# Performance work log

Measured on AMD Instinct MI355X. Metric: run time of the kernel, lower is better.

Reference implementation:

```python
import jax, jax.numpy as jnp
import numpy as np

WINDOW = 16  # hardcoded in module __init__

B, S, E, H = 2, 2048, 1024, 16
HD = E // H


def setup_inputs() -> dict:
    key = jax.random.key(0)
    k1, k2, k3, k4, k5, k6 = jax.random.split(key, 6)
    input_embeddings = jax.random.normal(k1, (B, S, E), dtype=jnp.float32)
    token_ids = jax.random.randint(k2, (B, S), 0, 32000, dtype=jnp.int64)
    # nn.MultiheadAttention parameters: packed in_proj (3E, E) + bias, out_proj (E, E) + bias
    in_proj_weight = jax.random.normal(k3, (3 * E, E), dtype=jnp.float32) * 0.02
    in_proj_bias = jax.random.normal(k4, (3 * E,), dtype=jnp.float32) * 0.02
    out_proj_weight = jax.random.normal(k5, (E, E), dtype=jnp.float32) * 0.02
    out_proj_bias = jax.random.normal(k6, (E,), dtype=jnp.float32) * 0.02
    return {
        "input_embeddings": input_embeddings,
        "token_ids": token_ids,
        "in_proj_weight": in_proj_weight,
        "in_proj_bias": in_proj_bias,
        "out_proj_weight": out_proj_weight,
        "out_proj_bias": out_proj_bias,
    }


def _blocked_mask(seq_len: int) -> jnp.ndarray:
    # Module sets mask[i, j] = True for j in [i - WINDOW, i] (17 positions).
    # PyTorch bool attn_mask: True = NOT allowed to attend.
    i = jnp.arange(seq_len)[:, None]
    j = jnp.arange(seq_len)[None, :]
    return (j <= i) & (j >= i - WINDOW)  # [S, S] bool, True = masked out


def reference(input_embeddings, token_ids, in_proj_weight, in_proj_bias,
              out_proj_weight, out_proj_bias):
    x = input_embeddings  # [B, S, E]
    b, s, e = x.shape
    # Packed QKV projection (torch Linear: y = x W^T + b)
    qkv = jnp.einsum('bse,fe->bsf', x, in_proj_weight) + in_proj_bias  # [B, S, 3E]
    q, k, v = jnp.split(qkv, 3, axis=-1)
    # Split heads: [B, H, S, HD]
    q = q.reshape(b, s, H, HD).transpose(0, 2, 1, 3)
    k = k.reshape(b, s, H, HD).transpose(0, 2, 1, 3)
    v = v.reshape(b, s, H, HD).transpose(0, 2, 1, 3)
    scale = 1.0 / jnp.sqrt(jnp.asarray(HD, dtype=x.dtype))
    scores = jnp.einsum('bhqd,bhkd->bhqk', q * scale, k)  # [B, H, S, S]
    blocked = _blocked_mask(s)  # True = masked
    scores = jnp.where(blocked[None, None, :, :], -jnp.inf, scores)
    attn = jax.nn.softmax(scores, axis=-1)
    ctx = jnp.einsum('bhqk,bhkd->bhqd', attn, v)  # [B, H, S, HD]
    ctx = ctx.transpose(0, 2, 1, 3).reshape(b, s, e)
    out = jnp.einsum('bse,fe->bsf', ctx, out_proj_weight) + out_proj_bias
    return out
```

## Files before the change

### kernel.cpp

```cpp
#include <hip/hip_runtime.h>

typedef __attribute__((ext_vector_type(8))) __bf16 bf16x8;
typedef __attribute__((ext_vector_type(4))) float f32x4;
typedef __attribute__((ext_vector_type(16))) float f32x16;
typedef unsigned short u16;
typedef unsigned int u32;

#define MFMA16(a, b, c) __builtin_amdgcn_mfma_f32_16x16x32_bf16((a), (b), (c), 0, 0, 0)
#define MFMA32(a, b, c) __builtin_amdgcn_mfma_f32_32x32x16_bf16((a), (b), (c), 0, 0, 0)

__device__ __forceinline__ u16 f2bf(float f) {
  return (u16)((__float_as_uint(f) + 0x8000u) >> 16);
}

#define BDIM 2
#define SDIM 2048
#define EDIM 1024
#define HDIM 16
#define HD 64
#define MDIM (BDIM * SDIM)

#define SC_C1 0.1803368801111355f

typedef __attribute__((address_space(3))) void lds_void;
typedef __attribute__((address_space(1))) void g_void;

__device__ __forceinline__ void async_lds16(const void* g, void* lds_byte) {
  __builtin_amdgcn_global_load_lds((const g_void*)g, (lds_void*)lds_byte, 16, 0, 0);
}

__global__ __launch_bounds__(256) void cvt3_kernel(
    const float* __restrict__ s0, u16* __restrict__ d0, int n0,
    const float* __restrict__ s1, u16* __restrict__ d1, int n1,
    const float* __restrict__ s2, u16* __restrict__ d2, int n2) {
  int i = (blockIdx.x * 256 + threadIdx.x) * 8;
  const float* s;
  u16* d;
  if (i < n0) {
    s = s0 + i; d = d0 + i;
  } else if (i < n0 + n1) {
    s = s1 + (i - n0); d = d1 + (i - n0);
  } else if (i < n0 + n1 + n2) {
    s = s2 + (i - n0 - n1); d = d2 + (i - n0 - n1);
  } else {
    return;
  }
  float4 f0 = *(const float4*)(s);
  float4 f1 = *(const float4*)(s + 4);
  union { uint4 u; u16 h[8]; } o;
  o.h[0] = f2bf(f0.x); o.h[1] = f2bf(f0.y); o.h[2] = f2bf(f0.z); o.h[3] = f2bf(f0.w);
  o.h[4] = f2bf(f1.x); o.h[5] = f2bf(f1.y); o.h[6] = f2bf(f1.z); o.h[7] = f2bf(f1.w);
  *(uint4*)(d) = o.u;
}

__global__ __launch_bounds__(256) void gemm_qkv_kernel(
    const u16* __restrict__ X, const u16* __restrict__ W,
    const float* __restrict__ bias, u16* __restrict__ qb,
    u16* __restrict__ kb, u16* __restrict__ vtb) {
  __shared__ __align__(16) u16 As[128 * 64];
  __shared__ __align__(16) u16 Bs[128 * 64];
  const int m0 = blockIdx.x * 128, n0 = blockIdx.y * 128;
  const bool isV = (n0 >= 2 * EDIM);
  const int t = threadIdx.x;
  const int l = t & 63;
  const int quad = l >> 4, col = l & 15;
  const int wid = t >> 6;
  const int mh = wid & 1, nh = wid >> 1;
  const int wofs = (t & 192) << 4;
  f32x4 acc[4][4] = {};
  const u16* Ab = X + (size_t)m0 * EDIM;
  const u16* Bb = W + (size_t)n0 * EDIM;
  char* AsB = (char*)As;
  char* BsB = (char*)Bs;

  for (int k0 = 0; k0 < EDIM; k0 += 64) {
    __syncthreads();
#pragma unroll
    for (int p = 0; p < 4; p++) {
      int idx = p * 256 + t;
      int row = idx >> 3;
      int gch = (idx & 7) ^ (row & 7);
      async_lds16(Ab + (size_t)row * EDIM + k0 + gch * 8, AsB + p * 4096 + wofs);
      async_lds16(Bb + (size_t)row * EDIM + k0 + gch * 8, BsB + p * 4096 + wofs);
    }
    __syncthreads();
#pragma unroll
    for (int kk = 0; kk < 2; kk++) {
      bf16x8 af[4], bfr[4];
#pragma unroll
      for (int i = 0; i < 4; i++) {
        int ra = 64 * mh + 16 * i + col;
        af[i] = *(const bf16x8*)&As[ra * 64 + (((kk * 4 + quad) ^ (ra & 7)) * 8)];
        int rb = 64 * nh + 16 * i + col;
        bfr[i] = *(const bf16x8*)&Bs[rb * 64 + (((kk * 4 + quad) ^ (rb & 7)) * 8)];
      }
      if (isV) {
#pragma unroll
        for (int i = 0; i < 4; i++)
#pragma unroll
          for (int j = 0; j < 4; j++)
            acc[i][j] = MFMA16(bfr[i], af[j], acc[i][j]);
      } else {
#pragma unroll
        for (int i = 0; i < 4; i++)
#pragma unroll
          for (int j = 0; j < 4; j++)
            acc[i][j] = MFMA16(af[i], bfr[j], acc[i][j]);
      }
    }
  }

  if (isV) {
#pragma unroll
    for (int i = 0; i < 4; i++)
#pragma unroll
      for (int j = 0; j < 4; j++)
#pragma unroll
        for (int r = 0; r < 4; r++) {
          int n = n0 + 64 * nh + 16 * i + quad * 4 + r;
          int m = m0 + 64 * mh + 16 * j + col;
          float val = acc[i][j][r] + bias[n];
          int e = n & 1023;
          int hh = e >> 6, d = e & 63;
          int bb = m >> 11, s = m & 2047;
          vtb[(((size_t)(bb * HDIM + hh)) * HD + d) * SDIM + s] = f2bf(val);
        }
  } else {
    const float qscale = (n0 < EDIM) ? SC_C1 : 1.0f;
#pragma unroll
    for (int i = 0; i < 4; i++)
#pragma unroll
      for (int j = 0; j < 4; j++)
#pragma unroll
        for (int r = 0; r < 4; r++) {
          int m = m0 + 64 * mh + 16 * i + quad * 4 + r;
          int n = n0 + 64 * nh + 16 * j + col;
          float val = (acc[i][j][r] + bias[n]) * qscale;
          int which = n >> 10, e = n & 1023;
          int hh = e >> 6, d = e & 63;
          int bb = m >> 11, s = m & 2047;
          u16* dst = (which == 0) ? qb : kb;
          dst[(((size_t)(bb * HDIM + hh)) * SDIM + s) * HD + d] = f2bf(val);
        }
  }
}

__global__ __launch_bounds__(256) void attn_kernel(
    const u16* __restrict__ qg, const u16* __restrict__ kg,
    const u16* __restrict__ vtg, u16* __restrict__ ctx) {
  __shared__ __align__(16) u16 KB[2][64 * 64];
  __shared__ __align__(16) u16 VB[3][64 * 64];

  const int bh = blockIdx.x;
  const int q0 = blockIdx.y * 128;
  const int t = threadIdx.x;
  const int wid = t >> 6, l = t & 63;
  const int col = l & 31, half = l >> 5;
  const size_t base = (size_t)bh * SDIM * HD;

  const int qw0 = q0 + 32 * wid;
  const int qi = qw0 + col;

  bf16x8 bq[4];
  {
    const u16* qp = qg + base + (size_t)qi * HD + half * 8;
#pragma unroll
    for (int f = 0; f < 4; f++) bq[f] = *(const bf16x8*)(qp + f * 16);
  }
  asm volatile("" : "+v"(bq[0]), "+v"(bq[1]), "+v"(bq[2]), "+v"(bq[3]));

  const int srow = t >> 3;
  const int g = (t & 7) ^ (srow & 7);
  const u16* kptr = kg + base + (size_t)srow * HD + g * 8;
  const u16* vptr = vtg + base + (size_t)srow * SDIM + g * 8;
  const int wofs = (t & 192) << 4;

  auto stageK = [&](int kt, int buf) {
    char* d = (char*)KB[buf] + wofs;
    async_lds16(kptr + (size_t)(kt * 64) * HD, d);
    async_lds16(kptr + (size_t)(kt * 64 + 32) * HD, d + 4096);
  };
  auto stageV = [&](int kt, int buf) {
    char* d = (char*)VB[buf] + wofs;
    async_lds16(vptr + kt * 64, d);
    async_lds16(vptr + (size_t)32 * SDIM + kt * 64, d + 4096);
  };

  auto qkt = [&](const u16* Kt, f32x16 (&sco)[2]) {
#pragma unroll
    for (int s = 0; s < 2; s++)
#pragma unroll
      for (int f = 0; f < 4; f++) {
        int kr = 32 * s + col;
        int phys = (2 * f + half) ^ (kr & 7);
        bf16x8 kf = *(const bf16x8*)&Kt[kr * 64 + phys * 8];
        sco[s] = MFMA32(kf, bq[f], sco[s]);
      }
  };

  float ps0 = 0.f, ps1 = 0.f, ps2 = 0.f, ps3 = 0.f;
  f32x16 oacc[2] = {};

  auto smax = [&](int kt, f32x16 (&cur)[2], bool band, u32 (&w)[2][8]) {
#pragma unroll
    for (int s = 0; s < 2; s++) {
      float p[16];
#pragma unroll
      for (int r = 0; r < 16; r++) {
        float v = cur[s][r];
        if (band) {
          int j = kt * 64 + 32 * s + (r & 3) + 8 * (r >> 2) + 4 * half;
          if (j <= qi && j + 16 >= qi) v = -1.0e30f;
        }
        p[r] = __builtin_exp2f(v);
      }
#pragma unroll
      for (int r = 0; r < 16; r++) {
        if ((r & 3) == 0) ps0 += p[r];
        else if ((r & 3) == 1) ps1 += p[r];
        else if ((r & 3) == 2) ps2 += p[r];
        else ps3 += p[r];
      }
#pragma unroll
      for (int j = 0; j < 8; j++) {
        u32 wv;
        asm("v_cvt_pk_bf16_f32 %0, %1, %2" : "=v"(wv) : "v"(p[2 * j]), "v"(p[2 * j + 1]));
        w[s][j] = wv;
      }
    }
  };

  auto pv = [&](const u16* Vt, u32 (&w)[2][8]) {
#pragma unroll
    for (int s = 0; s < 2; s++)
#pragma unroll
      for (int b2 = 0; b2 < 2; b2++) {
        u32 x0 = w[s][4 * b2 + 0], x1 = w[s][4 * b2 + 1];
        u32 y0 = w[s][4 * b2 + 2], y1 = w[s][4 * b2 + 3];
        asm("v_permlane32_swap_b32 %0, %1" : "+v"(x0), "+v"(y0));
        asm("v_permlane32_swap_b32 %0, %1" : "+v"(x1), "+v"(y1));
        uint4 pw;
        pw.x = x0; pw.y = x1; pw.z = y0; pw.w = y1;
        bf16x8 pa = __builtin_bit_cast(bf16x8, pw);
        int ks = 2 * s + b2;
#pragma unroll
        for (int dt = 0; dt < 2; dt++) {
          int vr = 32 * dt + col;
          int phys = (2 * ks + half) ^ (vr & 7);
          bf16x8 vf = *(const bf16x8*)&Vt[vr * 64 + phys * 8];
          oacc[dt] = MFMA32(vf, pa, oacc[dt]);
        }
      }
  };

  const int NT = SDIM / 64;

  auto body = [&](int kt, f32x16 (&cur)[2], f32x16 (&nxt)[2]) {
    __syncthreads();
    if (kt + 1 < NT) {
      nxt[0] = (f32x16){};
      nxt[1] = (f32x16){};
      qkt(KB[(kt + 1) & 1], nxt);
    }
    if (kt + 2 < NT) {
      stageK(kt + 2, kt & 1);
      stageV(kt + 2, (unsigned)(kt + 2) % 3u);
    }
    u32 w[2][8];
    bool band = (kt * 64 <= qw0 + 31) && (kt * 64 + 63 >= qw0 - 16);
    smax(kt, cur, band, w);
    pv(VB[(unsigned)kt % 3u], w);
  };

  f32x16 scA[2] = {}, scB[2] = {};
  stageK(0, 0);
  stageV(0, 0);
  __syncthreads();
  qkt(KB[0], scA);
  stageK(1, 1);
  stageV(1, 1);

#pragma unroll 1
  for (int kt = 0; kt < NT; kt += 2) {
    body(kt, scA, scB);
    body(kt + 1, scB, scA);
  }

  float psum = (ps0 + ps1) + (ps2 + ps3);
  psum += __shfl_xor(psum, 32, 64);
  float linv = 1.0f / psum;

  const int b = bh >> 4, h = bh & 15;
  u16* cbase = ctx + ((size_t)(b * SDIM + qi)) * EDIM + h * HD;
#pragma unroll
  for (int dt = 0; dt < 2; dt++)
#pragma unroll
    for (int a = 0; a < 4; a++) {
      float v0 = oacc[dt][4 * a + 0] * linv, v1 = oacc[dt][4 * a + 1] * linv;
      float v2 = oacc[dt][4 * a + 2] * linv, v3 = oacc[dt][4 * a + 3] * linv;
      u32 w0, w1;
      asm("v_cvt_pk_bf16_f32 %0, %1, %2" : "=v"(w0) : "v"(v0), "v"(v1));
      asm("v_cvt_pk_bf16_f32 %0, %1, %2" : "=v"(w1) : "v"(v2), "v"(v3));
      uint2 st;
      st.x = w0; st.y = w1;
      *(uint2*)(cbase + 32 * dt + 8 * a + 4 * half) = st;
    }
}

__global__ __launch_bounds__(256) void gemm_out_kernel(
    const u16* __restrict__ A, const u16* __restrict__ W,
    const float* __restrict__ bias, float* __restrict__ out) {
  __shared__ __align__(16) u16 As[128 * 64];
  __shared__ __align__(16) u16 Bs[128 * 64];
  const int m0 = blockIdx.x * 128, n0 = blockIdx.y * 128;
  const int t = threadIdx.x;
  const int l = t & 63;
  const int quad = l >> 4, col = l & 15;
  const int wid = t >> 6;
  const int mh = wid & 1, nh = wid >> 1;
  const int wofs = (t & 192) << 4;
  f32x4 acc[4][4] = {};
  const u16* Ab = A + (size_t)m0 * EDIM;
  const u16* Bb = W + (size_t)n0 * EDIM;
  char* AsB = (char*)As;
  char* BsB = (char*)Bs;

  for (int k0 = 0; k0 < EDIM; k0 += 64) {
    __syncthreads();
#pragma unroll
    for (int p = 0; p < 4; p++) {
      int idx = p * 256 + t;
      int row = idx >> 3;
      int gch = (idx & 7) ^ (row & 7);
      async_lds16(Ab + (size_t)row * EDIM + k0 + gch * 8, AsB + p * 4096 + wofs);
      async_lds16(Bb + (size_t)row * EDIM + k0 + gch * 8, BsB + p * 4096 + wofs);
    }
    __syncthreads();
#pragma unroll
    for (int kk = 0; kk < 2; kk++) {
      bf16x8 af[4], bfr[4];
#pragma unroll
      for (int i = 0; i < 4; i++) {
        int ra = 64 * mh + 16 * i + col;
        af[i] = *(const bf16x8*)&As[ra * 64 + (((kk * 4 + quad) ^ (ra & 7)) * 8)];
        int rb = 64 * nh + 16 * i + col;
        bfr[i] = *(const bf16x8*)&Bs[rb * 64 + (((kk * 4 + quad) ^ (rb & 7)) * 8)];
      }
#pragma unroll
      for (int i = 0; i < 4; i++)
#pragma unroll
        for (int j = 0; j < 4; j++)
          acc[i][j] = MFMA16(af[i], bfr[j], acc[i][j]);
    }
  }

#pragma unroll
  for (int i = 0; i < 4; i++)
#pragma unroll
    for (int j = 0; j < 4; j++)
#pragma unroll
      for (int r = 0; r < 4; r++) {
        int m = m0 + 64 * mh + 16 * i + quad * 4 + r;
        int n = n0 + 64 * nh + 16 * j + col;
        out[(size_t)m * EDIM + n] = acc[i][j][r] + bias[n];
      }
}

extern "C" void kernel_launch(void* const* d_in, const int* in_sizes, int n_in,
                              void* d_out, int out_size, void* d_ws,
                              size_t ws_size, hipStream_t stream) {
  const float* x = (const float*)d_in[0];
  const float* in_w = (const float*)d_in[2];
  const float* in_b = (const float*)d_in[3];
  const float* out_w = (const float*)d_in[4];
  const float* out_b = (const float*)d_in[5];
  float* out = (float*)d_out;

  char* ws = (char*)d_ws;
  u16* Xb  = (u16*)ws;
  u16* ctx = (u16*)ws;
  u16* qb  = (u16*)(ws + (size_t)( 8 << 20));
  u16* kb  = (u16*)(ws + (size_t)(16 << 20));
  u16* vtb = (u16*)(ws + (size_t)(24 << 20));
  u16* Wib = (u16*)(ws + (size_t)(32 << 20));
  u16* Wob = (u16*)(ws + (size_t)(38 << 20));

  const int nX = MDIM * EDIM;
  const int nWi = 3 * EDIM * EDIM;
  const int nWo = EDIM * EDIM;
  cvt3_kernel<<<(nX + nWi + nWo) / 8 / 256, 256, 0, stream>>>(
      x, Xb, nX, in_w, Wib, nWi, out_w, Wob, nWo);

  gemm_qkv_kernel<<<dim3(MDIM / 128, 3 * EDIM / 128), 256, 0, stream>>>(
      Xb, Wib, in_b, qb, kb, vtb);
  attn_kernel<<<dim3(BDIM * HDIM, SDIM / 128), 256, 0, stream>>>(qb, kb, vtb, ctx);
  gemm_out_kernel<<<dim3(MDIM / 128, EDIM / 128), 256, 0, stream>>>(
      ctx, Wob, out_b, out);
}
```

Measured before the change: 219.7 us.

## Split attention key tiles across wave pairs, halving query rows per block

Each attention block now covers 64 query rows instead of 128. The four waves split into two query groups times two key halves, so each wave computes one 32-key sub-tile per step, and partial outputs and row sums are reduced through LDS at the end. This doubles the grid to raise occupancy and shortens per-wave work. Plain __syncthreads are replaced by explicit vmcnt waits and barriers, and s_setprio is added around the MFMA sections. The cost is twice as many K/V tile loads per query row plus an extra LDS reduction and barrier.

```diff
diff --git a/kernel.cpp b/kernel.cpp
--- a/kernel.cpp
+++ b/kernel.cpp
@@ -145,20 +145,22 @@
   }
 }
 
-__global__ __launch_bounds__(256) void attn_kernel(
+__global__ __launch_bounds__(256, 4) void attn_kernel(
     const u16* __restrict__ qg, const u16* __restrict__ kg,
     const u16* __restrict__ vtg, u16* __restrict__ ctx) {
   __shared__ __align__(16) u16 KB[2][64 * 64];
   __shared__ __align__(16) u16 VB[3][64 * 64];
 
   const int bh = blockIdx.x;
-  const int q0 = blockIdx.y * 128;
+  const int q0 = blockIdx.y * 64;
   const int t = threadIdx.x;
   const int wid = t >> 6, l = t & 63;
   const int col = l & 31, half = l >> 5;
+  const int wq = wid & 1;
+  const int kh = wid >> 1;
   const size_t base = (size_t)bh * SDIM * HD;
 
-  const int qw0 = q0 + 32 * wid;
+  const int qw0 = q0 + 32 * wq;
   const int qi = qw0 + col;
 
   bf16x8 bq[4];
@@ -169,116 +171,118 @@
   }
   asm volatile("" : "+v"(bq[0]), "+v"(bq[1]), "+v"(bq[2]), "+v"(bq[3]));
 
-  const int srow = t >> 3;
-  const int g = (t & 7) ^ (srow & 7);
-  const u16* kptr = kg + base + (size_t)srow * HD + g * 8;
-  const u16* vptr = vtg + base + (size_t)srow * SDIM + g * 8;
-  const int wofs = (t & 192) << 4;
+  const int sr = l >> 3;
+  const int g = (l & 7) ^ sr;
+  const u16* kpt = kg + base + (size_t)(16 * wid + sr) * HD + g * 8;
+  const u16* vpt = vtg + base + (size_t)(16 * wid + sr) * SDIM + g * 8;
 
   auto stageK = [&](int kt, int buf) {
-    char* d = (char*)KB[buf] + wofs;
-    async_lds16(kptr + (size_t)(kt * 64) * HD, d);
-    async_lds16(kptr + (size_t)(kt * 64 + 32) * HD, d + 4096);
+    char* d = (char*)KB[buf] + wid * 2048;
+    async_lds16(kpt + (size_t)(kt * 64) * HD, d);
+    async_lds16(kpt + (size_t)(kt * 64 + 8) * HD, d + 1024);
   };
   auto stageV = [&](int kt, int buf) {
-    char* d = (char*)VB[buf] + wofs;
-    async_lds16(vptr + kt * 64, d);
-    async_lds16(vptr + (size_t)32 * SDIM + kt * 64, d + 4096);
-  };
-
-  auto qkt = [&](const u16* Kt, f32x16 (&sco)[2]) {
-#pragma unroll
-    for (int s = 0; s < 2; s++)
-#pragma unroll
-      for (int f = 0; f < 4; f++) {
-        int kr = 32 * s + col;
-        int phys = (2 * f + half) ^ (kr & 7);
-        bf16x8 kf = *(const bf16x8*)&Kt[kr * 64 + phys * 8];
-        sco[s] = MFMA32(kf, bq[f], sco[s]);
-      }
+    char* d = (char*)VB[buf] + wid * 2048;
+    async_lds16(vpt + kt * 64, d);
+    async_lds16(vpt + (size_t)8 * SDIM + kt * 64, d + 1024);
+  };
+
+  auto qkt = [&](const u16* Kt, f32x16& sco) {
+    const int kr = 32 * kh + col;
+    const int r7 = kr & 7;
+#pragma unroll
+    for (int f = 0; f < 4; f++) {
+      int phys = (2 * f + half) ^ r7;
+      bf16x8 kf = *(const bf16x8*)&Kt[kr * 64 + phys * 8];
+      sco = MFMA32(kf, bq[f], sco);
+    }
   };
 
   float ps0 = 0.f, ps1 = 0.f, ps2 = 0.f, ps3 = 0.f;
   f32x16 oacc[2] = {};
 
-  auto smax = [&](int kt, f32x16 (&cur)[2], bool band, u32 (&w)[2][8]) {
-#pragma unroll
-    for (int s = 0; s < 2; s++) {
-      float p[16];
-#pragma unroll
-      for (int r = 0; r < 16; r++) {
-        float v = cur[s][r];
-        if (band) {
-          int j = kt * 64 + 32 * s + (r & 3) + 8 * (r >> 2) + 4 * half;
-          if (j <= qi && j + 16 >= qi) v = -1.0e30f;
-        }
-        p[r] = __builtin_exp2f(v);
-      }
-#pragma unroll
-      for (int r = 0; r < 16; r++) {
-        if ((r & 3) == 0) ps0 += p[r];
-        else if ((r & 3) == 1) ps1 += p[r];
-        else if ((r & 3) == 2) ps2 += p[r];
-        else ps3 += p[r];
-      }
-#pragma unroll
-      for (int j = 0; j < 8; j++) {
-        u32 wv;
-        asm("v_cvt_pk_bf16_f32 %0, %1, %2" : "=v"(wv) : "v"(p[2 * j]), "v"(p[2 * j + 1]));
-        w[s][j] = wv;
-      }
-    }
-  };
-
-  auto pv = [&](const u16* Vt, u32 (&w)[2][8]) {
-#pragma unroll
-    for (int s = 0; s < 2; s++)
-#pragma unroll
-      for (int b2 = 0; b2 < 2; b2++) {
-        u32 x0 = w[s][4 * b2 + 0], x1 = w[s][4 * b2 + 1];
-        u32 y0 = w[s][4 * b2 + 2], y1 = w[s][4 * b2 + 3];
-        asm("v_permlane32_swap_b32 %0, %1" : "+v"(x0), "+v"(y0));
-        asm("v_permlane32_swap_b32 %0, %1" : "+v"(x1), "+v"(y1));
-        uint4 pw;
-        pw.x = x0; pw.y = x1; pw.z = y0; pw.w = y1;
-        bf16x8 pa = __builtin_bit_cast(bf16x8, pw);
-        int ks = 2 * s + b2;
-#pragma unroll
-        for (int dt = 0; dt < 2; dt++) {
-          int vr = 32 * dt + col;
-          int phys = (2 * ks + half) ^ (vr & 7);
-          bf16x8 vf = *(const bf16x8*)&Vt[vr * 64 + phys * 8];
-          oacc[dt] = MFMA32(vf, pa, oacc[dt]);
-        }
-      }
+  auto smax = [&](int kt, f32x16& cur, bool band, u32 (&w)[8]) {
+    float p[16];
+#pragma unroll
+    for (int r = 0; r < 16; r++) {
+      float v = cur[r];
+      if (band) {
+        int j = kt * 64 + 32 * kh + (r & 3) + 8 * (r >> 2) + 4 * half;
+        if (j <= qi && j + 16 >= qi) v = -1.0e30f;
+      }
+      p[r] = __builtin_exp2f(v);
+    }
+#pragma unroll
+    for (int r = 0; r < 16; r += 4) {
+      ps0 += p[r]; ps1 += p[r + 1]; ps2 += p[r + 2]; ps3 += p[r + 3];
+    }
+#pragma unroll
+    for (int j = 0; j < 8; j++)
+      asm("v_cvt_pk_bf16_f32 %0, %1, %2"
+          : "=v"(w[j]) : "v"(p[2 * j]), "v"(p[2 * j + 1]));
+  };
+
+  auto pv = [&](const u16* Vt, u32 (&w)[8]) {
+#pragma unroll
+    for (int b2 = 0; b2 < 2; b2++) {
+      u32 x0 = w[4 * b2 + 0], x1 = w[4 * b2 + 1];
+      u32 y0 = w[4 * b2 + 2], y1 = w[4 * b2 + 3];
+      asm("v_permlane32_swap_b32 %0, %1" : "+v"(x0), "+v"(y0));
+      asm("v_permlane32_swap_b32 %0, %1" : "+v"(x1), "+v"(y1));
+      uint4 pw;
+      pw.x = x0; pw.y = x1; pw.z = y0; pw.w = y1;
+      bf16x8 pa = __builtin_bit_cast(bf16x8, pw);
+      int ks = 2 * kh + b2;
+#pragma unroll
+      for (int dt = 0; dt < 2; dt++) {
+        int vr = 32 * dt + col;
+        int phys = (2 * ks + half) ^ (vr & 7);
+        bf16x8 vf = *(const bf16x8*)&Vt[vr * 64 + phys * 8];
+        oacc[dt] = MFMA32(vf, pa, oacc[dt]);
+      }
+    }
   };
 
   const int NT = SDIM / 64;
-
-  auto body = [&](int kt, f32x16 (&cur)[2], f32x16 (&nxt)[2]) {
-    __syncthreads();
-    if (kt + 1 < NT) {
-      nxt[0] = (f32x16){};
-      nxt[1] = (f32x16){};
-      qkt(KB[(kt + 1) & 1], nxt);
-    }
+  int vcur = 0, vstg = 2;
+
+  auto body = [&](int kt, f32x16& cur, f32x16& nxt) {
+    if (kt < NT - 1)
+      asm volatile("s_waitcnt vmcnt(2) lgkmcnt(0)" ::: "memory");
+    else
+      asm volatile("s_waitcnt vmcnt(0) lgkmcnt(0)" ::: "memory");
+    __builtin_amdgcn_s_barrier();
+    __builtin_amdgcn_sched_barrier(0);
     if (kt + 2 < NT) {
       stageK(kt + 2, kt & 1);
-      stageV(kt + 2, (unsigned)(kt + 2) % 3u);
-    }
-    u32 w[2][8];
-    bool band = (kt * 64 <= qw0 + 31) && (kt * 64 + 63 >= qw0 - 16);
+      stageV(kt + 2, vstg);
+    }
+    if (kt + 1 < NT) {
+      nxt = (f32x16){};
+      __builtin_amdgcn_s_setprio(1);
+      qkt(KB[(kt + 1) & 1], nxt);
+      __builtin_amdgcn_s_setprio(0);
+    }
+    u32 w[8];
+    bool band = (kt * 64 + 32 * kh <= qw0 + 31) &&
+                (kt * 64 + 32 * kh + 31 >= qw0 - 16);
     smax(kt, cur, band, w);
-    pv(VB[(unsigned)kt % 3u], w);
-  };
-
-  f32x16 scA[2] = {}, scB[2] = {};
+    __builtin_amdgcn_s_setprio(1);
+    pv(VB[vcur], w);
+    __builtin_amdgcn_s_setprio(0);
+    vcur = (vcur == 2) ? 0 : vcur + 1;
+    vstg = (vstg == 2) ? 0 : vstg + 1;
+  };
+
+  f32x16 scA = {}, scB = {};
   stageK(0, 0);
   stageV(0, 0);
-  __syncthreads();
-  qkt(KB[0], scA);
   stageK(1, 1);
   stageV(1, 1);
+  asm volatile("s_waitcnt vmcnt(6)" ::: "memory");
+  __builtin_amdgcn_s_barrier();
+  __builtin_amdgcn_sched_barrier(0);
+  qkt(KB[0], scA);
 
 #pragma unroll 1
   for (int kt = 0; kt < NT; kt += 2) {
@@ -286,25 +290,47 @@
     body(kt + 1, scB, scA);
   }
 
-  float psum = (ps0 + ps1) + (ps2 + ps3);
-  psum += __shfl_xor(psum, 32, 64);
-  float linv = 1.0f / psum;
-
-  const int b = bh >> 4, h = bh & 15;
-  u16* cbase = ctx + ((size_t)(b * SDIM + qi)) * EDIM + h * HD;
-#pragma unroll
-  for (int dt = 0; dt < 2; dt++)
-#pragma unroll
-    for (int a = 0; a < 4; a++) {
-      float v0 = oacc[dt][4 * a + 0] * linv, v1 = oacc[dt][4 * a + 1] * linv;
-      float v2 = oacc[dt][4 * a + 2] * linv, v3 = oacc[dt][4 * a + 3] * linv;
-      u32 w0, w1;
-      asm("v_cvt_pk_bf16_f32 %0, %1, %2" : "=v"(w0) : "v"(v0), "v"(v1));
-      asm("v_cvt_pk_bf16_f32 %0, %1, %2" : "=v"(w1) : "v"(v2), "v"(v3));
-      uint2 st;
-      st.x = w0; st.y = w1;
-      *(uint2*)(cbase + 32 * dt + 8 * a + 4 * half) = st;
-    }
+  float pst = (ps0 + ps1) + (ps2 + ps3);
+  pst += __shfl_xor(pst, 32, 64);
+  __syncthreads();
+  char* EXO = (char*)VB;
+  float* EXP = (float*)((char*)VB + 16384);
+  if (kh == 1) {
+#pragma unroll
+    for (int c = 0; c < 8; c++) {
+      f32x4 part;
+#pragma unroll
+      for (int m = 0; m < 4; m++) part[m] = oacc[c >> 2][4 * (c & 3) + m];
+      *(f32x4*)(EXO + wq * 8192 + l * 128 + ((c ^ (l & 7)) << 4)) = part;
+    }
+    if (l < 32) EXP[wq * 32 + l] = pst;
+  }
+  __syncthreads();
+  if (kh == 0) {
+    float linv = 1.0f / (pst + EXP[wq * 32 + col]);
+#pragma unroll
+    for (int c = 0; c < 8; c++) {
+      f32x4 part = *(const f32x4*)(EXO + wq * 8192 + l * 128 + ((c ^ (l & 7)) << 4));
+#pragma unroll
+      for (int m = 0; m < 4; m++) oacc[c >> 2][4 * (c & 3) + m] += part[m];
+    }
+    const int b = bh >> 4, h = bh & 15;
+    u16* cbase = ctx + ((size_t)(b * SDIM + qi)) * EDIM + h * HD;
+#pragma unroll
+    for (int dt = 0; dt < 2; dt++)
+#pragma unroll
+      for (int a = 0; a < 4; a++) {
+        float v0 = oacc[dt][4 * a + 0] * linv, v1 = oacc[dt][4 * a + 1] * linv;
+        float v2 = oacc[dt][4 * a + 2] * linv, v3 = oacc[dt][4 * a + 3] * linv;
+        u32 w0, w1;
+        asm("v_cvt_pk_bf16_f32 %0, %1, %2" : "=v"(w0) : "v"(v0), "v"(v1));
+        asm("v_cvt_pk_bf16_f32 %0, %1, %2" : "=v"(w1) : "v"(v2), "v"(v3));
+        uint2 st;
+        st.x = w0;
+        st.y = w1;
+        *(uint2*)(cbase + 32 * dt + 8 * a + 4 * half) = st;
+      }
+  }
 }
 
 __global__ __launch_bounds__(256) void gemm_out_kernel(
@@ -393,7 +419,7 @@
 
   gemm_qkv_kernel<<<dim3(MDIM / 128, 3 * EDIM / 128), 256, 0, stream>>>(
       Xb, Wib, in_b, qb, kb, vtb);
-  attn_kernel<<<dim3(BDIM * HDIM, SDIM / 128), 256, 0, stream>>>(qb, kb, vtb, ctx);
+  attn_kernel<<<dim3(BDIM * HDIM, SDIM / 64), 256, 0, stream>>>(qb, kb, vtb, ctx);
   gemm_out_kernel<<<dim3(MDIM / 128, EDIM / 128), 256, 0, stream>>>(
       ctx, Wob, out_b, out);
 }
```

Result: slower. 242.3 us (+10.3%).

## Restructure attention loop to process two K/V tiles per barrier with 4-deep buffers

Applied to the files above, without the earlier changes.

Reworks the attention main loop so each iteration stages two future K/V tiles and computes QK^T, softmax and PV for two tiles between a single __syncthreads, using 4-slot K and V LDS buffers instead of 2/3. This halves the barrier count and groups the MFMA work for better ILP. In exchange it drops the software-pipelined overlap of next-tile QK^T with the current softmax, raises LDS use per block (which may lower occupancy), and holds two score accumulators live at once, raising register pressure.

```diff
diff --git a/kernel.cpp b/kernel.cpp
--- a/kernel.cpp
+++ b/kernel.cpp
@@ -148,8 +148,8 @@
 __global__ __launch_bounds__(256) void attn_kernel(
     const u16* __restrict__ qg, const u16* __restrict__ kg,
     const u16* __restrict__ vtg, u16* __restrict__ ctx) {
-  __shared__ __align__(16) u16 KB[2][64 * 64];
-  __shared__ __align__(16) u16 VB[3][64 * 64];
+  __shared__ __align__(16) u16 KB[4][64 * 64];
+  __shared__ __align__(16) u16 VB[4][64 * 64];
 
   const int bh = blockIdx.x;
   const int q0 = blockIdx.y * 128;
@@ -255,35 +255,35 @@
 
   const int NT = SDIM / 64;
 
-  auto body = [&](int kt, f32x16 (&cur)[2], f32x16 (&nxt)[2]) {
-    __syncthreads();
-    if (kt + 1 < NT) {
-      nxt[0] = (f32x16){};
-      nxt[1] = (f32x16){};
-      qkt(KB[(kt + 1) & 1], nxt);
-    }
-    if (kt + 2 < NT) {
-      stageK(kt + 2, kt & 1);
-      stageV(kt + 2, (unsigned)(kt + 2) % 3u);
-    }
-    u32 w[2][8];
-    bool band = (kt * 64 <= qw0 + 31) && (kt * 64 + 63 >= qw0 - 16);
-    smax(kt, cur, band, w);
-    pv(VB[(unsigned)kt % 3u], w);
-  };
-
-  f32x16 scA[2] = {}, scB[2] = {};
   stageK(0, 0);
   stageV(0, 0);
-  __syncthreads();
-  qkt(KB[0], scA);
   stageK(1, 1);
   stageV(1, 1);
 
+  f32x16 scA[2], scB[2];
 #pragma unroll 1
-  for (int kt = 0; kt < NT; kt += 2) {
-    body(kt, scA, scB);
-    body(kt + 1, scB, scA);
+  for (int s = 0; s < NT / 2; s++) {
+    const int a = 2 * s, b = a + 1;
+    __syncthreads();
+    if (s < NT / 2 - 1) {
+      stageK(a + 2, (a + 2) & 3);
+      stageV(a + 2, (a + 2) & 3);
+      stageK(b + 2, (b + 2) & 3);
+      stageV(b + 2, (b + 2) & 3);
+    }
+    scA[0] = (f32x16){};
+    scA[1] = (f32x16){};
+    qkt(KB[a & 3], scA);
+    scB[0] = (f32x16){};
+    scB[1] = (f32x16){};
+    qkt(KB[b & 3], scB);
+    u32 wA[2][8], wB[2][8];
+    const bool bandA = (a * 64 <= qw0 + 31) && (a * 64 + 63 >= qw0 - 16);
+    smax(a, scA, bandA, wA);
+    pv(VB[a & 3], wA);
+    const bool bandB = (b * 64 <= qw0 + 31) && (b * 64 + 63 >= qw0 - 16);
+    smax(b, scB, bandB, wB);
+    pv(VB[b & 3], wB);
   }
 
   float psum = (ps0 + ps1) + (ps2 + ps3);
```

Result: slower. 225.1 us (+2.4%).
